# Kernel optimization log

Hardware: AMD Instinct MI355X
Metric: run time of the kernel (lower is better)

Reference implementation:

```python
import jax, jax.numpy as jnp
import numpy as np

KH, KW = 3, 3
STRIDE = (1, 1)
PAD = 1


def _patches(x):
    # x: (B, C, H, W) -> (B, C, KH, KW, OH, OW)
    B, C, H, W = x.shape
    p = jax.lax.conv_general_dilated_patches(
        x, filter_shape=(KH, KW), window_strides=STRIDE,
        padding=[(PAD, PAD), (PAD, PAD)],
        dimension_numbers=('NCHW', 'OIHW', 'NCHW'))
    OH, OW = p.shape[2], p.shape[3]
    # feature dim of patches is ordered (C, KH, KW) — channel-major
    return p.reshape(B, C, KH, KW, OH, OW)


def setup_inputs() -> dict:
    key = jax.random.key(0)
    k1, k2 = jax.random.split(key, 2)
    B, C, H, W, O = 8, 32, 64, 64, 32
    OH = (H - KH + 2 * PAD) // STRIDE[0] + 1
    OW = (W - KW + 2 * PAD) // STRIDE[1] + 1
    x = jax.random.normal(k1, (B, C, H, W), dtype=jnp.float32)
    # xavier_uniform on the 6D weight (torch fan-in/out convention):
    recf = O * C * KH * KW
    fan_in, fan_out = OW * recf, OH * recf
    limit = float(np.sqrt(6.0 / (fan_in + fan_out)))
    weights = jax.random.uniform(k2, (OH, OW, O, C, KH, KW),
                                 minval=-limit, maxval=limit,
                                 dtype=jnp.float32)
    bias = jnp.zeros((O,), dtype=jnp.float32)
    return {"x": x, "weights": weights, "bias": bias}


def reference(x, weights, bias):
    # locally connected 2D conv: unique weight per output location.
    p = _patches(x)  # (B, C, KH, KW, OH, OW)
    # Faithful to the torch einsum 'bchw,ocwh->bo': the weight's kernel
    # spatial dims (kH,kW) are labeled (w,h), i.e. spatially transposed
    # relative to the patch.
    out = jnp.einsum('bchwij,ijocwh->boij', p, weights)
    return out + bias[None, :, None, None]
```

## Files before the change

kernel.cpp:

```cpp
#include <hip/hip_runtime.h>


#define NB 8
#define NC 32
#define NO 32
#define NH 64
#define NW 64
#define KK 288
#define LOCS 8
#define XCOLS 10
#define XNAT_SZ (NB * NC * 3 * XCOLS)

typedef __attribute__((ext_vector_type(8))) short s16x8;
typedef __attribute__((ext_vector_type(4))) float f32x4;

union Frag {
  unsigned int u[4];
  unsigned short s[8];
  uint4 q;
  s16x8 v;
};

__device__ __forceinline__ unsigned short f2bf(float f) {
  unsigned int u = __float_as_uint(f);
  u += 0x7FFFu + ((u >> 16) & 1u);
  return (unsigned short)(u >> 16);
}

__global__ __launch_bounds__(256, 2) void lc2d_kernel(
    const float* __restrict__ x, const float* __restrict__ w,
    const float* __restrict__ bias, float* __restrict__ out) {
  const int bid = blockIdx.x;
  const int g = (bid & 7) * 64 + (bid >> 3);
  const int loc0 = g * LOCS;
  const int i = loc0 >> 6;
  const int j0 = loc0 & 63;
  const int t = threadIdx.x;
  const int lane = t & 63;
  const int wv = t >> 6;
  const int m16 = lane & 15;
  const int kg = lane >> 4;

  __shared__ float xnat[XNAT_SZ];
  __shared__ unsigned int xtb[LOCS * 9 * 32 * 4];
  __shared__ float obuf[LOCS * NB * NO];

#pragma unroll
  for (int it = 0; it < 30; ++it) {
    int e = t + it * 256;
    int row = e / XCOLS;
    int cc = e - row * XCOLS;
    int bc = row / 3;
    int yy = row - bc * 3;
    int y = i + yy - 1;
    int xc = j0 + cc - 1;
    float v = 0.f;
    if ((unsigned)y < 64u && (unsigned)xc < 64u)
      v = x[(bc * NH + y) * NW + xc];
    xnat[e] = v;
  }
  asm volatile("" ::: "memory");

  float4 wb[2][18];
  {
    const int lloc = 2 * wv;
    const float* wp0 = w + (((size_t)(loc0 + lloc) * NO) + 0 * 16 + m16) * KK + kg * 8;
    const float* wp1 = w + (((size_t)(loc0 + lloc) * NO) + 1 * 16 + m16) * KK + kg * 8;
#pragma unroll
    for (int ks = 0; ks < 9; ++ks) {
      wb[0][2 * ks]     = *(const float4*)(wp0 + ks * 32);
      wb[0][2 * ks + 1] = *(const float4*)(wp0 + ks * 32 + 4);
      wb[1][2 * ks]     = *(const float4*)(wp1 + ks * 32);
      wb[1][2 * ks + 1] = *(const float4*)(wp1 + ks * 32 + 4);
    }
  }
  asm volatile("s_waitcnt lgkmcnt(0)\n\ts_barrier" ::: "memory");

  {
    const int bl = t >> 5;
    const int idx = t & 31;
    const int bkg = idx >> 3;
    const int bm = idx & 7;
#pragma unroll
    for (int ks = 0; ks < 9; ++ks) {
      Frag f;
#pragma unroll
      for (int e = 0; e < 8; ++e) {
        int k = ks * 32 + bkg * 8 + e;
        int c = k / 9;
        int rem = k - c * 9;
        int a = rem / 3;
        int bb = rem - a * 3;
        f.s[e] = f2bf(xnat[((bm * NC + c) * 3 + bb) * XCOLS + bl + a]);
      }
      *(uint4*)&xtb[((bl * 9 + ks) * 32 + idx) * 4] = f.q;
    }
  }
  asm volatile("s_waitcnt lgkmcnt(0)\n\ts_barrier" ::: "memory");

  uint4 afr[9];
  auto load_a = [&](int lloc) {
#pragma unroll
    for (int ks = 0; ks < 9; ++ks) {
      if (m16 < 8)
        afr[ks] = *(const uint4*)&xtb[((lloc * 9 + ks) * 32 + kg * 8 + m16) * 4];
      else
        afr[ks] = make_uint4(0, 0, 0, 0);
    }
  };

#pragma unroll
  for (int p = 0; p < 4; ++p) {
    const int lp = p >> 1;
    const int ot = p & 1;
    const int lloc = 2 * wv + lp;
    if (ot == 0) load_a(lloc);

    const int nlloc = 2 * wv + 1;
    const float* wpn = w + (((size_t)(loc0 + nlloc) * NO) + p * 16 + m16) * KK + kg * 8;

    f32x4 acc = {0.f, 0.f, 0.f, 0.f};
#pragma unroll
    for (int ks = 0; ks < 9; ++ks) {
      float4 lo = wb[p & 1][2 * ks];
      float4 hi = wb[p & 1][2 * ks + 1];
      Frag fb;
      fb.s[0] = f2bf(lo.x); fb.s[1] = f2bf(lo.y);
      fb.s[2] = f2bf(lo.z); fb.s[3] = f2bf(lo.w);
      fb.s[4] = f2bf(hi.x); fb.s[5] = f2bf(hi.y);
      fb.s[6] = f2bf(hi.z); fb.s[7] = f2bf(hi.w);
      Frag fa; fa.q = afr[ks];
      acc = __builtin_amdgcn_mfma_f32_16x16x32_bf16(fa.v, fb.v, acc, 0, 0, 0);
      if (p < 2) {
        wb[p & 1][2 * ks]     = *(const float4*)(wpn + ks * 32);
        wb[p & 1][2 * ks + 1] = *(const float4*)(wpn + ks * 32 + 4);
      }
    }

    if (kg < 2) {
#pragma unroll
      for (int r = 0; r < 4; ++r) {
        int row = kg * 4 + r;
        obuf[(lloc * NB + row) * NO + ot * 16 + m16] = acc[r];
      }
    }
  }
  asm volatile("s_waitcnt lgkmcnt(0)\n\ts_barrier" ::: "memory");

  {
    const int fb_ = t >> 5;
    const int fo = t & 31;
    const float bia = bias[fo];
    float4 r0, r1;
    r0.x = obuf[(0 * NB + fb_) * NO + fo] + bia;
    r0.y = obuf[(1 * NB + fb_) * NO + fo] + bia;
    r0.z = obuf[(2 * NB + fb_) * NO + fo] + bia;
    r0.w = obuf[(3 * NB + fb_) * NO + fo] + bia;
    r1.x = obuf[(4 * NB + fb_) * NO + fo] + bia;
    r1.y = obuf[(5 * NB + fb_) * NO + fo] + bia;
    r1.z = obuf[(6 * NB + fb_) * NO + fo] + bia;
    r1.w = obuf[(7 * NB + fb_) * NO + fo] + bia;
    float* op = &out[((size_t)(fb_ * NO + fo) * NH + i) * NW + j0];
    *(float4*)op = r0;
    *(float4*)(op + 4) = r1;
  }
}

extern "C" void kernel_launch(void* const* d_in, const int* in_sizes, int n_in,
                              void* d_out, int out_size, void* d_ws, size_t ws_size,
                              hipStream_t stream) {
  const float* x    = (const float*)d_in[0];
  const float* w    = (const float*)d_in[1];
  const float* bias = (const float*)d_in[2];
  float* out = (float*)d_out;
  lc2d_kernel<<<dim3(NH * NW / LOCS), dim3(256), 0, stream>>>(x, w, bias, out);
}
```

Baseline: 40.00 us.

## Shrink per-block work to two locations and raise occupancy for more parallelism

Each block now covers 2 output locations instead of 8, giving four times as many blocks. Each wave computes a single location times 16-output tile, which removes the in-register weight prefetch pipeline, and launch bounds now allow 4 blocks per CU. The aim is more concurrent blocks and more weight bytes in flight to hide memory latency on this bandwidth-bound weight stream. The cost is more redundant halo loads of x per block and more per-block setup and barrier overhead; the bf16 conversion also switches to the HIP intrinsic.

New measurement: 33.76 us, median of 2. 15.6% less time.

```diff
diff --git a/kernel.cpp b/kernel.cpp
--- a/kernel.cpp
+++ b/kernel.cpp
@@ -1,4 +1,5 @@
 #include <hip/hip_runtime.h>
+#include <hip/hip_bf16.h>
 
 
 #define NB 8
@@ -7,31 +8,27 @@
 #define NH 64
 #define NW 64
 #define KK 288
-#define LOCS 8
-#define XCOLS 10
-#define XNAT_SZ (NB * NC * 3 * XCOLS)
+#define LOCS 2
+#define XCOLS 4
+#define NROWS (NB * NC * 3)
+#define XNAT_SZ (NROWS * XCOLS)
+#define NSLOT (LOCS * 9 * 32)
 
 typedef __attribute__((ext_vector_type(8))) short s16x8;
 typedef __attribute__((ext_vector_type(4))) float f32x4;
 
-union Frag {
-  unsigned int u[4];
-  unsigned short s[8];
-  uint4 q;
-  s16x8 v;
-};
+union Frag { unsigned short s[8]; uint4 q; s16x8 v; };
 
 __device__ __forceinline__ unsigned short f2bf(float f) {
-  unsigned int u = __float_as_uint(f);
-  u += 0x7FFFu + ((u >> 16) & 1u);
-  return (unsigned short)(u >> 16);
+  __hip_bfloat16 h = __float2bfloat16(f);
+  return *reinterpret_cast<unsigned short*>(&h);
 }
 
-__global__ __launch_bounds__(256, 2) void lc2d_kernel(
+__global__ __launch_bounds__(256, 4) void lc2d_kernel(
     const float* __restrict__ x, const float* __restrict__ w,
     const float* __restrict__ bias, float* __restrict__ out) {
   const int bid = blockIdx.x;
-  const int g = (bid & 7) * 64 + (bid >> 3);
+  const int g = (bid & 7) * 256 + (bid >> 3);
   const int loc0 = g * LOCS;
   const int i = loc0 >> 6;
   const int j0 = loc0 & 63;
@@ -40,16 +37,19 @@
   const int wv = t >> 6;
   const int m16 = lane & 15;
   const int kg = lane >> 4;
+  const int l = wv >> 1;
+  const int ot = wv & 1;
 
   __shared__ float xnat[XNAT_SZ];
-  __shared__ unsigned int xtb[LOCS * 9 * 32 * 4];
-  __shared__ float obuf[LOCS * NB * NO];
+  __shared__ uint4 xtb[NSLOT];
+  __shared__ float obuf[LOCS][NB][NO];
 
+  float sv[12];
 #pragma unroll
-  for (int it = 0; it < 30; ++it) {
+  for (int it = 0; it < 12; ++it) {
     int e = t + it * 256;
-    int row = e / XCOLS;
-    int cc = e - row * XCOLS;
+    int row = e >> 2;
+    int cc = e & 3;
     int bc = row / 3;
     int yy = row - bc * 3;
     int y = i + yy - 1;
@@ -57,112 +57,79 @@
     float v = 0.f;
     if ((unsigned)y < 64u && (unsigned)xc < 64u)
       v = x[(bc * NH + y) * NW + xc];
-    xnat[e] = v;
+    sv[it] = v;
   }
-  asm volatile("" ::: "memory");
 
-  float4 wb[2][18];
+  float4 wf[18];
   {
-    const int lloc = 2 * wv;
-    const float* wp0 = w + (((size_t)(loc0 + lloc) * NO) + 0 * 16 + m16) * KK + kg * 8;
-    const float* wp1 = w + (((size_t)(loc0 + lloc) * NO) + 1 * 16 + m16) * KK + kg * 8;
+    const float* wp =
+        w + ((size_t)(loc0 + l) * NO + ot * 16 + m16) * KK + kg * 8;
 #pragma unroll
     for (int ks = 0; ks < 9; ++ks) {
-      wb[0][2 * ks]     = *(const float4*)(wp0 + ks * 32);
-      wb[0][2 * ks + 1] = *(const float4*)(wp0 + ks * 32 + 4);
-      wb[1][2 * ks]     = *(const float4*)(wp1 + ks * 32);
-      wb[1][2 * ks + 1] = *(const float4*)(wp1 + ks * 32 + 4);
+      wf[2 * ks]     = *(const float4*)(wp + ks * 32);
+      wf[2 * ks + 1] = *(const float4*)(wp + ks * 32 + 4);
     }
+  }
+
+#pragma unroll
+  for (int it = 0; it < 12; ++it) xnat[t + it * 256] = sv[it];
+  asm volatile("s_waitcnt lgkmcnt(0)\n\ts_barrier" ::: "memory");
+
+  for (int sid = t; sid < NSLOT; sid += 256) {
+    int l2 = sid / 288;
+    int r = sid - l2 * 288;
+    int ks = r >> 5;
+    int idx = r & 31;
+    int bkg = idx >> 3;
+    int bm = idx & 7;
+    Frag f;
+#pragma unroll
+    for (int e = 0; e < 8; ++e) {
+      int k = ks * 32 + bkg * 8 + e;
+      int c = k / 9;
+      int rem = k - c * 9;
+      int a = rem / 3;
+      int bb = rem - a * 3;
+      f.s[e] = f2bf(xnat[((bm * NC + c) * 3 + bb) * XCOLS + l2 + a]);
+    }
+    xtb[sid] = f.q;
+  }
+  asm volatile("s_waitcnt lgkmcnt(0)\n\ts_barrier" ::: "memory");
+
+  uint4 afr[9];
+#pragma unroll
+  for (int ks = 0; ks < 9; ++ks)
+    afr[ks] = xtb[(l * 9 + ks) * 32 + kg * 8 + (m16 & 7)];
+
+  f32x4 acc = {0.f, 0.f, 0.f, 0.f};
+#pragma unroll
+  for (int ks = 0; ks < 9; ++ks) {
+    float4 lo = wf[2 * ks], hi = wf[2 * ks + 1];
+    Frag fb;
+    fb.s[0] = f2bf(lo.x); fb.s[1] = f2bf(lo.y);
+    fb.s[2] = f2bf(lo.z); fb.s[3] = f2bf(lo.w);
+    fb.s[4] = f2bf(hi.x); fb.s[5] = f2bf(hi.y);
+    fb.s[6] = f2bf(hi.z); fb.s[7] = f2bf(hi.w);
+    Frag fa; fa.q = afr[ks];
+    acc = __builtin_amdgcn_mfma_f32_16x16x32_bf16(fa.v, fb.v, acc, 0, 0, 0);
+  }
+
+  if (kg < 2) {
+#pragma unroll
+    for (int r = 0; r < 4; ++r)
+      obuf[l][kg * 4 + r][ot * 16 + m16] = acc[r];
   }
   asm volatile("s_waitcnt lgkmcnt(0)\n\ts_barrier" ::: "memory");
 
   {
-    const int bl = t >> 5;
-    const int idx = t & 31;
-    const int bkg = idx >> 3;
-    const int bm = idx & 7;
-#pragma unroll
-    for (int ks = 0; ks < 9; ++ks) {
-      Frag f;
-#pragma unroll
-      for (int e = 0; e < 8; ++e) {
-        int k = ks * 32 + bkg * 8 + e;
-        int c = k / 9;
-        int rem = k - c * 9;
-        int a = rem / 3;
-        int bb = rem - a * 3;
-        f.s[e] = f2bf(xnat[((bm * NC + c) * 3 + bb) * XCOLS + bl + a]);
-      }
-      *(uint4*)&xtb[((bl * 9 + ks) * 32 + idx) * 4] = f.q;
-    }
-  }
-  asm volatile("s_waitcnt lgkmcnt(0)\n\ts_barrier" ::: "memory");
-
-  uint4 afr[9];
-  auto load_a = [&](int lloc) {
-#pragma unroll
-    for (int ks = 0; ks < 9; ++ks) {
-      if (m16 < 8)
-        afr[ks] = *(const uint4*)&xtb[((lloc * 9 + ks) * 32 + kg * 8 + m16) * 4];
-      else
-        afr[ks] = make_uint4(0, 0, 0, 0);
-    }
-  };
-
-#pragma unroll
-  for (int p = 0; p < 4; ++p) {
-    const int lp = p >> 1;
-    const int ot = p & 1;
-    const int lloc = 2 * wv + lp;
-    if (ot == 0) load_a(lloc);
-
-    const int nlloc = 2 * wv + 1;
-    const float* wpn = w + (((size_t)(loc0 + nlloc) * NO) + p * 16 + m16) * KK + kg * 8;
-
-    f32x4 acc = {0.f, 0.f, 0.f, 0.f};
-#pragma unroll
-    for (int ks = 0; ks < 9; ++ks) {
-      float4 lo = wb[p & 1][2 * ks];
-      float4 hi = wb[p & 1][2 * ks + 1];
-      Frag fb;
-      fb.s[0] = f2bf(lo.x); fb.s[1] = f2bf(lo.y);
-      fb.s[2] = f2bf(lo.z); fb.s[3] = f2bf(lo.w);
-      fb.s[4] = f2bf(hi.x); fb.s[5] = f2bf(hi.y);
-      fb.s[6] = f2bf(hi.z); fb.s[7] = f2bf(hi.w);
-      Frag fa; fa.q = afr[ks];
-      acc = __builtin_amdgcn_mfma_f32_16x16x32_bf16(fa.v, fb.v, acc, 0, 0, 0);
-      if (p < 2) {
-        wb[p & 1][2 * ks]     = *(const float4*)(wpn + ks * 32);
-        wb[p & 1][2 * ks + 1] = *(const float4*)(wpn + ks * 32 + 4);
-      }
-    }
-
-    if (kg < 2) {
-#pragma unroll
-      for (int r = 0; r < 4; ++r) {
-        int row = kg * 4 + r;
-        obuf[(lloc * NB + row) * NO + ot * 16 + m16] = acc[r];
-      }
-    }
-  }
-  asm volatile("s_waitcnt lgkmcnt(0)\n\ts_barrier" ::: "memory");
-
-  {
-    const int fb_ = t >> 5;
-    const int fo = t & 31;
-    const float bia = bias[fo];
-    float4 r0, r1;
-    r0.x = obuf[(0 * NB + fb_) * NO + fo] + bia;
-    r0.y = obuf[(1 * NB + fb_) * NO + fo] + bia;
-    r0.z = obuf[(2 * NB + fb_) * NO + fo] + bia;
-    r0.w = obuf[(3 * NB + fb_) * NO + fo] + bia;
-    r1.x = obuf[(4 * NB + fb_) * NO + fo] + bia;
-    r1.y = obuf[(5 * NB + fb_) * NO + fo] + bia;
-    r1.z = obuf[(6 * NB + fb_) * NO + fo] + bia;
-    r1.w = obuf[(7 * NB + fb_) * NO + fo] + bia;
-    float* op = &out[((size_t)(fb_ * NO + fo) * NH + i) * NW + j0];
-    *(float4*)op = r0;
-    *(float4*)(op + 4) = r1;
+    const int b_ = t >> 5;
+    const int o_ = t & 31;
+    const float bia = bias[o_];
+    float2 r2;
+    r2.x = obuf[0][b_][o_] + bia;
+    r2.y = obuf[1][b_][o_] + bia;
+    *reinterpret_cast<float2*>(
+        &out[((size_t)(b_ * NO + o_) * NH + i) * NW + j0]) = r2;
   }
 }
 
```
